# Performance work log

Measured on AMD Instinct MI355X. Metric: run time of the kernel, lower is better.

The kernel has to match this reference:

```python
import jax, jax.numpy as jnp
import numpy as np

EPS = 1e-5
N_HEADS = 8

def layer_norm(x, g, b):
    mu = x.mean(-1, keepdims=True)
    var = ((x - mu) ** 2).mean(-1, keepdims=True)
    return (x - mu) * jax.lax.rsqrt(var + EPS) * g + b

def rotate_half(x):
    d = x.shape[-1] // 2
    return jnp.concatenate([-x[..., d:], x[..., :d]], axis=-1)

def setup_inputs() -> dict:
    key = jax.random.key(0)
    ks = jax.random.split(key, 6)
    b, n, m, h, dh = 4, 512, 8192, N_HEADS, 16
    dim = h * dh
    s = dim ** -0.5
    return {
        "x": jax.random.normal(ks[0], (b, n, dim), jnp.float32),
        "mem_kv": jax.random.normal(ks[1], (b, h, m, 2 * dh), jnp.float32),
        "w_q": jax.random.normal(ks[2], (dim, dim), jnp.float32) * s,
        "w_kv": jax.random.normal(ks[3], (2 * dim, dim), jnp.float32) * s,
        "w_out": jax.random.normal(ks[4], (dim, dim), jnp.float32) * s,
        "b_out": jnp.zeros((dim,), jnp.float32),
        "g1": jnp.ones((dim,), jnp.float32),
        "b1": jnp.zeros((dim,), jnp.float32),
        "g2": jnp.ones((dim,), jnp.float32),
        "b2": jnp.zeros((dim,), jnp.float32),
    }

def reference(x, mem_kv, w_q, w_kv, w_out, b_out, g1, b1, g2, b2):
    b, n, dim = x.shape
    h = N_HEADS
    dh = dim // h
    # pre-norm + projections
    x_ = layer_norm(x, g1, b1)
    q = (x_ @ w_q.T).reshape(b, n, h, dh).transpose(0, 2, 1, 3)          # [b,h,n,dh]
    kv = (x_ @ w_kv.T).reshape(b, n, h, 2 * dh).transpose(0, 2, 1, 3)    # [b,h,n,2dh]
    mem_kv = jnp.concatenate([mem_kv, kv], axis=2)                        # growing cache
    k, v = jnp.split(mem_kv, 2, axis=-1)                                  # [b,h,j,dh] each
    q = q * dh ** -0.5
    # rotary embeddings (SinusoidalEmbeddings over k length, q uses trailing n positions)
    j = k.shape[2]
    inv_freq = 1.0 / (10000.0 ** (jnp.arange(0, dh, 2, dtype=jnp.float32) / dh))
    fr = jnp.arange(j, dtype=jnp.float32)[:, None] * inv_freq[None, :]
    freqs = jnp.concatenate([fr, fr], axis=-1)                            # [j, dh]
    cos, sin = jnp.cos(freqs), jnp.sin(freqs)
    q = q * cos[-n:] + rotate_half(q) * sin[-n:]
    k = k * cos + rotate_half(k) * sin
    # full attention of new chunk over cache (forward_simple, inference)
    sim = jnp.einsum('bhie,bhje->bhij', q, k)
    attn = jax.nn.softmax(sim, axis=-1)
    hv = jnp.einsum('bhij,bhje->bhie', attn, v)
    hv = hv.transpose(0, 2, 1, 3).reshape(b, n, dim) + x                  # residual
    out = layer_norm(hv, g2, b2) @ w_out.T + b_out + hv                   # out proj + residual
    return out, mem_kv
```

## Files before the change

### kernel.cpp

```cpp
#include <hip/hip_runtime.h>

#define B 4
#define N 512
#define M 8192
#define H 8
#define DH 16
#define DIM 128
#define J (M + N)
#define LN10000_DIV8 1.1512925465f
#define LOG2E 1.44269504f

typedef _Float16 f16;
typedef _Float16 half4 __attribute__((ext_vector_type(4)));
typedef _Float16 half8 __attribute__((ext_vector_type(8)));
typedef float f32x4 __attribute__((ext_vector_type(4)));

#define WS_KROT 0ull
#define WS_VT   8912896ull
#define WS_QROT 17825792ull
#define WS_HV   18350080ull
#define WS_XN   18874368ull

union K16 { f16 h[16]; uint4 u[2]; };
union V4  { f16 h[4];  uint2 u; };

__device__ __forceinline__ half8 cvt8(const float* p) {
    float4 a = *(const float4*)p, b = *(const float4*)(p + 4);
    half8 h = { (f16)a.x, (f16)a.y, (f16)a.z, (f16)a.w,
                (f16)b.x, (f16)b.y, (f16)b.z, (f16)b.w };
    return h;
}


__global__ void prep_kernel(const float4* __restrict__ src, float4* __restrict__ dst,
                            f16* __restrict__ krot, f16* __restrict__ vt,
                            const float* __restrict__ x, const float* __restrict__ g1,
                            const float* __restrict__ b1, f16* __restrict__ xn16)
{
    if (blockIdx.x < 4096) {
        __shared__ float tile[64][33];
        int bh = blockIdx.x >> 7;
        int j0 = (blockIdx.x & 127) * 64;
        int t = threadIdx.x;

        #pragma unroll
        for (int rep = 0; rep < 2; rep++) {
            int idx = t + rep * 256;
            int row = idx >> 3, c4 = idx & 7;
            float4 v = src[((size_t)bh * M + j0 + row) * 8 + c4];
            dst[((size_t)bh * J + j0 + row) * 8 + c4] = v;
            tile[row][c4 * 4 + 0] = v.x; tile[row][c4 * 4 + 1] = v.y;
            tile[row][c4 * 4 + 2] = v.z; tile[row][c4 * 4 + 3] = v.w;
        }
        __syncthreads();

        if (t < 64) {
            int j = j0 + t;
            K16 kr;
            #pragma unroll
            for (int r = 0; r < 8; r++) {
                float ang = (float)j * __expf(-(float)r * LN10000_DIV8);
                float sn, cs; __sincosf(ang, &sn, &cs);
                float lo = tile[t][r], hi = tile[t][r + 8];
                kr.h[r]     = (f16)(lo * cs - hi * sn);
                kr.h[r + 8] = (f16)(hi * cs + lo * sn);
            }
            int tilei = j >> 5, jj = j & 31;
            int col4 = (jj >> 3) * 4 + (jj & 3), frag = (jj >> 2) & 1;
            f16* base = krot + (size_t)bh * J * 16 + (size_t)tilei * 512 + col4 * 8 + frag * 4;
            #pragma unroll
            for (int q = 0; q < 4; q++) {
                V4 w;
                #pragma unroll
                for (int i = 0; i < 4; i++) w.h[i] = kr.h[q * 4 + i];
                *(uint2*)(base + q * 128) = w.u;
            }
        }
        {
            int dh = t >> 4, c0 = (t & 15) * 4;
            V4 vv;
            #pragma unroll
            for (int i = 0; i < 4; i++) vv.h[i] = (f16)tile[c0 + i][16 + dh];
            *(uint2*)(vt + (size_t)bh * 16 * J + (size_t)dh * J + j0 + c0) = vv.u;
        }
    } else {
        int wave = threadIdx.x >> 6, lane = threadIdx.x & 63;
        int token = (blockIdx.x - 4096) * 4 + wave;
        float v0 = x[(size_t)token * DIM + lane];
        float v1 = x[(size_t)token * DIM + lane + 64];
        float s = v0 + v1;
        for (int off = 32; off; off >>= 1) s += __shfl_xor(s, off, 64);
        float mu = s * (1.0f / DIM);
        float d0 = v0 - mu, d1 = v1 - mu;
        float vs = d0 * d0 + d1 * d1;
        for (int off = 32; off; off >>= 1) vs += __shfl_xor(vs, off, 64);
        float rs = rsqrtf(vs * (1.0f / DIM) + 1e-5f);
        xn16[(size_t)token * DIM + lane]      = (f16)(d0 * rs * g1[lane]      + b1[lane]);
        xn16[(size_t)token * DIM + lane + 64] = (f16)(d1 * rs * g1[lane + 64] + b1[lane + 64]);
    }
}

__global__ void __launch_bounds__(256) proj_kernel(
    const f16* __restrict__ xn16, const float* __restrict__ wq,
    const float* __restrict__ wkv, float* __restrict__ out_mem,
    f16* __restrict__ krot, f16* __restrict__ vt, f16* __restrict__ qrot)
{
    int id = blockIdx.x * 4 + (threadIdx.x >> 6);
    int lane = threadIdx.x & 63;
    int ttile = id & 127, ctile = id >> 7;
    int token0 = ttile * 16;
    int col = lane & 15, quad = lane >> 4;

    const float* wbase = (ctile < 8) ? (wq + (size_t)(ctile * 16 + col) * DIM)
                                     : (wkv + (size_t)((ctile - 8) * 16 + col) * DIM);
    const f16* abase = xn16 + (size_t)(token0 + col) * DIM + quad * 8;

    f32x4 acc = {0.f, 0.f, 0.f, 0.f};
    #pragma unroll
    for (int kb = 0; kb < 4; kb++) {
        half8 a = *(const half8*)(abase + kb * 32);
        half8 w = cvt8(wbase + kb * 32 + quad * 8);
        acc = __builtin_amdgcn_mfma_f32_16x16x32_f16(a, w, acc, 0, 0, 0);
    }

    int e = col, r8 = e & 7;
    float f = __expf(-(float)r8 * LN10000_DIV8);
    int kt = ctile - 8;
    int head = (ctile < 8) ? ctile : (kt >> 1);
    int isV  = (ctile >= 8) ? (kt & 1) : 0;

    #pragma unroll
    for (int r = 0; r < 4; r++) {
        int tok = token0 + quad * 4 + r;
        int b = tok >> 9, i = tok & (N - 1);
        int bhh = b * H + head;
        float self = acc[r];
        float prt = __shfl_xor(self, 8, 64);

        if (ctile < 8) {
            float ang = (float)(M + i) * f;
            float sn, cs; __sincosf(ang, &sn, &cs);
            float rv = (self * cs + ((e < 8) ? -prt : prt) * sn) * (0.25f * LOG2E);
            qrot[((size_t)bhh * N + i) * 16 + e] = (f16)rv;
        } else if (!isV) {
            out_mem[((size_t)bhh * J + M + i) * 32 + e] = self;
            float ang = (float)(M + i) * f;
            float sn, cs; __sincosf(ang, &sn, &cs);
            float rv = self * cs + ((e < 8) ? -prt : prt) * sn;
            int jpos = M + i;
            int tilei = jpos >> 5, jj = jpos & 31;
            int col4 = (jj >> 3) * 4 + (jj & 3), frag = (jj >> 2) & 1;
            krot[(size_t)bhh * J * 16 + (size_t)tilei * 512 +
                 (e >> 2) * 128 + col4 * 8 + frag * 4 + (e & 3)] = (f16)rv;
        } else {
            out_mem[((size_t)bhh * J + M + i) * 32 + 16 + e] = self;
            vt[(size_t)bhh * 16 * J + (size_t)e * J + M + i] = (f16)self;
        }
    }
}

__global__ void __launch_bounds__(512, 8) attn_kernel(
    const f16* __restrict__ krot, const f16* __restrict__ vt,
    const f16* __restrict__ qrot, f16* __restrict__ hvw)
{
    __shared__ float sacc[8][256];
    __shared__ float sl[8][16];
    int bh = blockIdx.x & 31;
    int q0 = (blockIdx.x >> 5) * 16;
    int wave = threadIdx.x >> 6, lane = threadIdx.x & 63;
    int col = lane & 15, quad = lane >> 4;

    const f16* vb = vt + (size_t)bh * 16 * J + (size_t)col * J;
    half4 qf = *(const half4*)(qrot + ((size_t)bh * N + q0 + col) * 16 + quad * 4);

    int jstart = wave * (J / 8);
    const f16* kptr = krot + (size_t)bh * J * 16 + (size_t)jstart * 16 + lane * 8;
    const f16* vptr = vb + jstart + quad * 8;

    f32x4 acc = {0.f, 0.f, 0.f, 0.f};
    const f32x4 zero = {0.f, 0.f, 0.f, 0.f};
    float lsum = 0.f;

    #pragma unroll 2
    for (int it = 0; it < 34; ++it) {
        half8 kf8 = *(const half8*)kptr;
        half8 vf  = *(const half8*)vptr;
        kptr += 512; vptr += 32;
        half4 kf0 = __builtin_shufflevector(kf8, kf8, 0, 1, 2, 3);
        half4 kf1 = __builtin_shufflevector(kf8, kf8, 4, 5, 6, 7);
        f32x4 s0 = __builtin_amdgcn_mfma_f32_16x16x16f16(kf0, qf, zero, 0, 0, 0);
        f32x4 s1 = __builtin_amdgcn_mfma_f32_16x16x16f16(kf1, qf, zero, 0, 0, 0);
        float p0 = exp2f(s0[0]), p1 = exp2f(s0[1]);
        float p2 = exp2f(s0[2]), p3 = exp2f(s0[3]);
        float p4 = exp2f(s1[0]), p5 = exp2f(s1[1]);
        float p6 = exp2f(s1[2]), p7 = exp2f(s1[3]);
        lsum += ((p0 + p1) + (p2 + p3)) + ((p4 + p5) + (p6 + p7));
        half8 pf = { (f16)p0, (f16)p1, (f16)p2, (f16)p3,
                     (f16)p4, (f16)p5, (f16)p6, (f16)p7 };
        acc = __builtin_amdgcn_mfma_f32_16x16x32_f16(pf, vf, acc, 0, 0, 0);
    }

    lsum += __shfl_xor(lsum, 16, 64);
    lsum += __shfl_xor(lsum, 32, 64);
    if (quad == 0) sl[wave][col] = lsum;
    #pragma unroll
    for (int r = 0; r < 4; r++) sacc[wave][(quad * 4 + r) * 16 + col] = acc[r];
    __syncthreads();

    if (wave == 0) {
        int b = bh >> 3, h = bh & 7;
        #pragma unroll
        for (int r = 0; r < 4; r++) {
            int ql = quad * 4 + r;
            float o = 0.f, lt = 0.f;
            #pragma unroll
            for (int w = 0; w < 8; w++) {
                o  += sacc[w][ql * 16 + col];
                lt += sl[w][ql];
            }
            hvw[((size_t)(b * N) + q0 + ql) * DIM + h * DH + col] = (f16)(o / lt);
        }
    }
}

__global__ void __launch_bounds__(256) final_kernel(
    const f16* __restrict__ hvw, const float* __restrict__ x,
    const float* __restrict__ wout, const float* __restrict__ bout,
    const float* __restrict__ g2, const float* __restrict__ b2v,
    float* __restrict__ out)
{
    __shared__ f16 xn2[16][136];
    __shared__ float hres[16][132];
    int token0 = blockIdx.x * 16;
    int wave = threadIdx.x >> 6, lane = threadIdx.x & 63;

    #pragma unroll
    for (int tt = 0; tt < 4; tt++) {
        int tl = wave * 4 + tt;
        int token = token0 + tl;
        float h0 = (float)hvw[(size_t)token * DIM + lane]      + x[(size_t)token * DIM + lane];
        float h1 = (float)hvw[(size_t)token * DIM + lane + 64] + x[(size_t)token * DIM + lane + 64];
        float s = h0 + h1;
        for (int off = 32; off; off >>= 1) s += __shfl_xor(s, off, 64);
        float mu = s * (1.0f / DIM);
        float d0 = h0 - mu, d1 = h1 - mu;
        float vs = d0 * d0 + d1 * d1;
        for (int off = 32; off; off >>= 1) vs += __shfl_xor(vs, off, 64);
        float rs = rsqrtf(vs * (1.0f / DIM) + 1e-5f);
        xn2[tl][lane]      = (f16)(d0 * rs * g2[lane]      + b2v[lane]);
        xn2[tl][lane + 64] = (f16)(d1 * rs * g2[lane + 64] + b2v[lane + 64]);
        hres[tl][lane] = h0; hres[tl][lane + 64] = h1;
    }
    __syncthreads();

    int col = lane & 15, quad = lane >> 4;
    #pragma unroll
    for (int cc = 0; cc < 2; cc++) {
        int ct = wave * 2 + cc;
        int cg = ct * 16 + col;
        const float* wrow = wout + (size_t)cg * DIM;
        f32x4 acc = {0.f, 0.f, 0.f, 0.f};
        #pragma unroll
        for (int kb = 0; kb < 4; kb++) {
            half8 a = *(const half8*)(&xn2[col][kb * 32 + quad * 8]);
            half8 w = cvt8(wrow + kb * 32 + quad * 8);
            acc = __builtin_amdgcn_mfma_f32_16x16x32_f16(a, w, acc, 0, 0, 0);
        }
        float bo = bout[cg];
        #pragma unroll
        for (int r = 0; r < 4; r++) {
            int tl = quad * 4 + r;
            out[(size_t)(token0 + tl) * DIM + cg] = acc[r] + bo + hres[tl][cg];
        }
    }
}

extern "C" void kernel_launch(void* const* d_in, const int* in_sizes, int n_in,
                              void* d_out, int out_size, void* d_ws, size_t ws_size,
                              hipStream_t stream)
{
    const float* x      = (const float*)d_in[0];
    const float* mem_kv = (const float*)d_in[1];
    const float* wq     = (const float*)d_in[2];
    const float* wkv    = (const float*)d_in[3];
    const float* wout   = (const float*)d_in[4];
    const float* bout   = (const float*)d_in[5];
    const float* g1     = (const float*)d_in[6];
    const float* b1     = (const float*)d_in[7];
    const float* g2     = (const float*)d_in[8];
    const float* b2     = (const float*)d_in[9];

    float* out = (float*)d_out;
    float* out_mem = out + (size_t)B * N * DIM;

    f16* krot = (f16*)((char*)d_ws + WS_KROT);
    f16* vt   = (f16*)((char*)d_ws + WS_VT);
    f16* qrot = (f16*)((char*)d_ws + WS_QROT);
    f16* hvw  = (f16*)((char*)d_ws + WS_HV);
    f16* xn16 = (f16*)((char*)d_ws + WS_XN);

    hipLaunchKernelGGL(prep_kernel, dim3(4608), dim3(256), 0, stream,
                       (const float4*)mem_kv, (float4*)out_mem, krot, vt,
                       x, g1, b1, xn16);
    hipLaunchKernelGGL(proj_kernel, dim3(768), dim3(256), 0, stream,
                       xn16, wq, wkv, out_mem, krot, vt, qrot);
    hipLaunchKernelGGL(attn_kernel, dim3(1024), dim3(512), 0, stream,
                       krot, vt, qrot, hvw);
    hipLaunchKernelGGL(final_kernel, dim3(128), dim3(256), 0, stream,
                       hvw, x, wout, bout, g2, b2, out);
}
```

Before: 160.2 us.

## Process two query tiles per attention block to reuse K/V loads

Each attention block now handles 32 queries (two 16-query tiles) instead of 16, so every K and V fragment loaded from global memory feeds two sets of MFMAs. The grid halves to 512 blocks and the launch-bounds occupancy hint drops from 8 to 4. The change also switches to the raw hardware exp2 builtin and packed round-toward-zero f16 conversion to cut ALU work in the softmax step. It costs more registers and shared memory per block and exposes less block-level parallelism, and the rtz conversion and unguarded exp2 slightly change numerics.

New measurement: 142.5 us. 1.12x faster.

```diff
diff --git a/kernel.cpp b/kernel.cpp
--- a/kernel.cpp
+++ b/kernel.cpp
@@ -13,7 +13,33 @@
 typedef _Float16 f16;
 typedef _Float16 half4 __attribute__((ext_vector_type(4)));
 typedef _Float16 half8 __attribute__((ext_vector_type(8)));
+typedef __fp16 fp16x2 __attribute__((ext_vector_type(2)));
 typedef float f32x4 __attribute__((ext_vector_type(4)));
+
+#if __has_builtin(__builtin_amdgcn_exp2f)
+#define EXP2(x) __builtin_amdgcn_exp2f(x)
+#else
+#define EXP2(x) exp2f(x)
+#endif
+
+union PK { fp16x2 v; unsigned int u; };
+
+__device__ __forceinline__ half8 pack8(float a, float b, float c, float d,
+                                       float e, float f, float g, float h) {
+#if __has_builtin(__builtin_amdgcn_cvt_pkrtz)
+    union { unsigned int u[4]; half8 h8; } r;
+    PK p0, p1, p2, p3;
+    p0.v = __builtin_amdgcn_cvt_pkrtz(a, b);
+    p1.v = __builtin_amdgcn_cvt_pkrtz(c, d);
+    p2.v = __builtin_amdgcn_cvt_pkrtz(e, f);
+    p3.v = __builtin_amdgcn_cvt_pkrtz(g, h);
+    r.u[0] = p0.u; r.u[1] = p1.u; r.u[2] = p2.u; r.u[3] = p3.u;
+    return r.h8;
+#else
+    half8 r = { (f16)a, (f16)b, (f16)c, (f16)d, (f16)e, (f16)f, (f16)g, (f16)h };
+    return r;
+#endif
+}
 
 #define WS_KROT 0ull
 #define WS_VT   8912896ull
@@ -30,7 +56,6 @@
                 (f16)b.x, (f16)b.y, (f16)b.z, (f16)b.w };
     return h;
 }
-
 
 __global__ void prep_kernel(const float4* __restrict__ src, float4* __restrict__ dst,
                             f16* __restrict__ krot, f16* __restrict__ vt,
@@ -159,27 +184,29 @@
     }
 }
 
-__global__ void __launch_bounds__(512, 8) attn_kernel(
+__global__ void __launch_bounds__(512, 4) attn_kernel(
     const f16* __restrict__ krot, const f16* __restrict__ vt,
     const f16* __restrict__ qrot, f16* __restrict__ hvw)
 {
-    __shared__ float sacc[8][256];
-    __shared__ float sl[8][16];
+    __shared__ float sacc[8][2][256];
+    __shared__ float sl[8][2][16];
     int bh = blockIdx.x & 31;
-    int q0 = (blockIdx.x >> 5) * 16;
+    int q0 = (blockIdx.x >> 5) * 32;
     int wave = threadIdx.x >> 6, lane = threadIdx.x & 63;
     int col = lane & 15, quad = lane >> 4;
 
     const f16* vb = vt + (size_t)bh * 16 * J + (size_t)col * J;
-    half4 qf = *(const half4*)(qrot + ((size_t)bh * N + q0 + col) * 16 + quad * 4);
+    half4 qfa = *(const half4*)(qrot + ((size_t)bh * N + q0 + col) * 16 + quad * 4);
+    half4 qfb = *(const half4*)(qrot + ((size_t)bh * N + q0 + 16 + col) * 16 + quad * 4);
 
     int jstart = wave * (J / 8);
     const f16* kptr = krot + (size_t)bh * J * 16 + (size_t)jstart * 16 + lane * 8;
     const f16* vptr = vb + jstart + quad * 8;
 
-    f32x4 acc = {0.f, 0.f, 0.f, 0.f};
+    f32x4 acca = {0.f, 0.f, 0.f, 0.f};
+    f32x4 accb = {0.f, 0.f, 0.f, 0.f};
     const f32x4 zero = {0.f, 0.f, 0.f, 0.f};
-    float lsum = 0.f;
+    float la = 0.f, lb = 0.f;
 
     #pragma unroll 2
     for (int it = 0; it < 34; ++it) {
@@ -188,26 +215,37 @@
         kptr += 512; vptr += 32;
         half4 kf0 = __builtin_shufflevector(kf8, kf8, 0, 1, 2, 3);
         half4 kf1 = __builtin_shufflevector(kf8, kf8, 4, 5, 6, 7);
-        f32x4 s0 = __builtin_amdgcn_mfma_f32_16x16x16f16(kf0, qf, zero, 0, 0, 0);
-        f32x4 s1 = __builtin_amdgcn_mfma_f32_16x16x16f16(kf1, qf, zero, 0, 0, 0);
-        float p0 = exp2f(s0[0]), p1 = exp2f(s0[1]);
-        float p2 = exp2f(s0[2]), p3 = exp2f(s0[3]);
-        float p4 = exp2f(s1[0]), p5 = exp2f(s1[1]);
-        float p6 = exp2f(s1[2]), p7 = exp2f(s1[3]);
-        lsum += ((p0 + p1) + (p2 + p3)) + ((p4 + p5) + (p6 + p7));
-        half8 pf = { (f16)p0, (f16)p1, (f16)p2, (f16)p3,
-                     (f16)p4, (f16)p5, (f16)p6, (f16)p7 };
-        acc = __builtin_amdgcn_mfma_f32_16x16x32_f16(pf, vf, acc, 0, 0, 0);
-    }
-
-    lsum += __shfl_xor(lsum, 16, 64);
-    lsum += __shfl_xor(lsum, 32, 64);
-    if (quad == 0) sl[wave][col] = lsum;
-    #pragma unroll
-    for (int r = 0; r < 4; r++) sacc[wave][(quad * 4 + r) * 16 + col] = acc[r];
+        f32x4 s0a = __builtin_amdgcn_mfma_f32_16x16x16f16(kf0, qfa, zero, 0, 0, 0);
+        f32x4 s1a = __builtin_amdgcn_mfma_f32_16x16x16f16(kf1, qfa, zero, 0, 0, 0);
+        f32x4 s0b = __builtin_amdgcn_mfma_f32_16x16x16f16(kf0, qfb, zero, 0, 0, 0);
+        f32x4 s1b = __builtin_amdgcn_mfma_f32_16x16x16f16(kf1, qfb, zero, 0, 0, 0);
+
+        float a0 = EXP2(s0a[0]), a1 = EXP2(s0a[1]), a2 = EXP2(s0a[2]), a3 = EXP2(s0a[3]);
+        float a4 = EXP2(s1a[0]), a5 = EXP2(s1a[1]), a6 = EXP2(s1a[2]), a7 = EXP2(s1a[3]);
+        float b0 = EXP2(s0b[0]), b1 = EXP2(s0b[1]), b2 = EXP2(s0b[2]), b3 = EXP2(s0b[3]);
+        float b4 = EXP2(s1b[0]), b5 = EXP2(s1b[1]), b6 = EXP2(s1b[2]), b7 = EXP2(s1b[3]);
+        la += ((a0 + a1) + (a2 + a3)) + ((a4 + a5) + (a6 + a7));
+        lb += ((b0 + b1) + (b2 + b3)) + ((b4 + b5) + (b6 + b7));
+        half8 pfa = pack8(a0, a1, a2, a3, a4, a5, a6, a7);
+        half8 pfb = pack8(b0, b1, b2, b3, b4, b5, b6, b7);
+        acca = __builtin_amdgcn_mfma_f32_16x16x32_f16(pfa, vf, acca, 0, 0, 0);
+        accb = __builtin_amdgcn_mfma_f32_16x16x32_f16(pfb, vf, accb, 0, 0, 0);
+    }
+
+    la += __shfl_xor(la, 16, 64);
+    la += __shfl_xor(la, 32, 64);
+    lb += __shfl_xor(lb, 16, 64);
+    lb += __shfl_xor(lb, 32, 64);
+    if (quad == 0) { sl[wave][0][col] = la; sl[wave][1][col] = lb; }
+    #pragma unroll
+    for (int r = 0; r < 4; r++) {
+        sacc[wave][0][(quad * 4 + r) * 16 + col] = acca[r];
+        sacc[wave][1][(quad * 4 + r) * 16 + col] = accb[r];
+    }
     __syncthreads();
 
-    if (wave == 0) {
+    if (wave < 2) {
+        int qt = wave;
         int b = bh >> 3, h = bh & 7;
         #pragma unroll
         for (int r = 0; r < 4; r++) {
@@ -215,10 +253,10 @@
             float o = 0.f, lt = 0.f;
             #pragma unroll
             for (int w = 0; w < 8; w++) {
-                o  += sacc[w][ql * 16 + col];
-                lt += sl[w][ql];
+                o  += sacc[w][qt][ql * 16 + col];
+                lt += sl[w][qt][ql];
             }
-            hvw[((size_t)(b * N) + q0 + ql) * DIM + h * DH + col] = (f16)(o / lt);
+            hvw[((size_t)(b * N) + q0 + qt * 16 + ql) * DIM + h * DH + col] = (f16)(o / lt);
         }
     }
 }
@@ -304,7 +342,7 @@
                        x, g1, b1, xn16);
     hipLaunchKernelGGL(proj_kernel, dim3(768), dim3(256), 0, stream,
                        xn16, wq, wkv, out_mem, krot, vt, qrot);
-    hipLaunchKernelGGL(attn_kernel, dim3(1024), dim3(512), 0, stream,
+    hipLaunchKernelGGL(attn_kernel, dim3(512), dim3(512), 0, stream,
                        krot, vt, qrot, hvw);
     hipLaunchKernelGGL(final_kernel, dim3(128), dim3(256), 0, stream,
                        hvw, x, wout, bout, g2, b2, out);
```
